# Kernel optimization log

Measured on AMD Instinct MI355X. Metric: run time of the kernel, lower is better.

Reference implementation:

```python
import jax, jax.numpy as jnp
import numpy as np

B, NV, NC, K = 2048, 1000, 4260, 3      # formulas, vars, clauses, literals/clause
NODES = 2 * NV + NC + 1                  # per-sample: pos lits | neg lits | clauses | root
N = B * NODES
C = B * NC


def setup_inputs() -> dict:
    key = jax.random.key(0)
    k1, k2 = jax.random.split(key)
    base = jnp.arange(B, dtype=jnp.int32) * NODES
    # positive / negative literal node ids (neg literal i is nv positions after pos literal i)
    pos_idx = (base[:, None] + jnp.arange(NV, dtype=jnp.int32)).ravel()
    neg_idx = pos_idx + NV
    # each clause picks K random literals from its own sample's 2*NV literal nodes
    lits = jax.random.randint(k1, (B, NC, K), 0, 2 * NV, dtype=jnp.int32)
    or_src = (lits + base[:, None, None]).ravel()              # [E] literal node per OR edge
    or_seg = jnp.repeat(jnp.arange(C, dtype=jnp.int32), K)     # [E] clause id per OR edge
    and_seg = jnp.repeat(jnp.arange(B, dtype=jnp.int32), NC)   # [C] root id per clause
    emb = jax.random.uniform(k2, (N,), dtype=jnp.float32)      # soft assignments in [0,1]
    return {"emb": emb, "pos_idx": pos_idx, "neg_idx": neg_idx,
            "or_src": or_src, "or_seg": or_seg, "and_seg": and_seg,
            "n_clauses": C, "n_roots": B, "epoch": 10}


def reference(emb, pos_idx, neg_idx, or_src, or_seg, and_seg, n_clauses, n_roots, epoch):
    t = jnp.asarray(epoch, jnp.float32) ** (-1.2)  # annealing temperature
    # literal transform: temporary[ind==1] = 1 - emb[ind==0]
    lit = emb.at[neg_idx].set(1.0 - emb[pos_idx])
    # --- OR gates: temperature-scaled soft-max over each clause's literals ---
    v = lit[or_src]                                            # [E] gathered literal values
    m = jax.ops.segment_max(v, or_seg, num_segments=n_clauses)
    w = jnp.exp((v - m[or_seg]) / t)                           # stabilized exp weights
    num = jax.ops.segment_sum(v * w, or_seg, num_segments=n_clauses)
    den = jax.ops.segment_sum(w, or_seg, num_segments=n_clauses)
    clause = num / den                                         # [C] soft-OR per clause
    # --- AND gate: temperature-scaled soft-min over each sample's clauses ---
    mn = jax.ops.segment_min(clause, and_seg, num_segments=n_roots)
    w2 = jnp.exp(-(clause - mn[and_seg]) / t)
    num2 = jax.ops.segment_sum(clause * w2, and_seg, num_segments=n_roots)
    den2 = jax.ops.segment_sum(w2, and_seg, num_segments=n_roots)
    return num2 / den2                                         # [B] soft-SAT per sample
```

## Files before the change

kernel.cpp:

```cpp
#include <hip/hip_runtime.h>

#define TPB 256

struct __align__(4) Int3 { int x, y, z; };

__global__ __launch_bounds__(TPB) void soft_sat_kernel(
    const float* __restrict__ emb,
    const int*   __restrict__ or_src,
    const int*   __restrict__ epoch_p,
    float* __restrict__ out,
    int NV, int NC, int NODES)
{
    extern __shared__ float smem[];
    float* lit = smem;
    float* cls = lit + 2 * NV;
    float* red = cls + NC;

    const int b     = blockIdx.x;
    const int tid   = threadIdx.x;
    const int lane  = tid & 63;
    const int wid   = tid >> 6;
    const int baseI = b * NODES;

    const float invt = powf((float)epoch_p[0], 1.2f);

    const float* embb = emb + baseI;
    for (int i = tid; i < NV; i += TPB) {
        float e = embb[i];
        lit[i]      = e;
        lit[i + NV] = 1.0f - e;
    }
    __syncthreads();

    const Int3* __restrict__ osb = (const Int3*)(or_src + (long long)b * NC * 3);
    float lmin = 3.4e38f;
    for (int c = tid; c < NC; c += TPB) {
        Int3 s = osb[c];
        float v0 = lit[s.x - baseI];
        float v1 = lit[s.y - baseI];
        float v2 = lit[s.z - baseI];
        float m  = fmaxf(fmaxf(v0, v1), v2);
        float w0 = __expf((v0 - m) * invt);
        float w1 = __expf((v1 - m) * invt);
        float w2 = __expf((v2 - m) * invt);
        float num = fmaf(v0, w0, fmaf(v1, w1, v2 * w2));
        float den = w0 + w1 + w2;
        float cv  = num / den;
        cls[c] = cv;
        lmin = fminf(lmin, cv);
    }

    for (int off = 32; off; off >>= 1) lmin = fminf(lmin, __shfl_xor(lmin, off));
    if (lane == 0) red[wid] = lmin;
    __syncthreads();
    if (tid == 0) {
        float m = red[0];
        for (int w = 1; w < TPB / 64; ++w) m = fminf(m, red[w]);
        red[0] = m;
    }
    __syncthreads();
    const float mn = red[0];
    __syncthreads();

    float n2 = 0.0f, d2 = 0.0f;
    for (int c = tid; c < NC; c += TPB) {
        float cv = cls[c];
        float w = __expf((mn - cv) * invt);
        n2 = fmaf(cv, w, n2);
        d2 += w;
    }
    for (int off = 32; off; off >>= 1) {
        n2 += __shfl_xor(n2, off);
        d2 += __shfl_xor(d2, off);
    }
    if (lane == 0) { red[wid] = n2; red[8 + wid] = d2; }
    __syncthreads();
    if (tid == 0) {
        float a = 0.0f, d = 0.0f;
        for (int w = 0; w < TPB / 64; ++w) { a += red[w]; d += red[8 + w]; }
        out[b] = a / d;
    }
}

extern "C" void kernel_launch(void* const* d_in, const int* in_sizes, int n_in,
                              void* d_out, int out_size, void* d_ws, size_t ws_size,
                              hipStream_t stream)
{
    const float* emb     = (const float*)d_in[0];
    const int*   or_src  = (const int*)d_in[3];
    const int*   epoch_p = (const int*)d_in[8];
    float*       out     = (float*)d_out;

    const int B     = out_size;
    const int NV    = in_sizes[1] / B;
    const int NODES = in_sizes[0] / B;
    const int C     = in_sizes[5];
    const int NC    = C / B;

    const size_t smem = (size_t)(2 * NV + NC + 16) * sizeof(float);
    soft_sat_kernel<<<B, TPB, smem, stream>>>(emb, or_src, epoch_p, out,
                                              NV, NC, NODES);
}
```

Measured before the change: 257.6 us.

## Fuse clause soft-OR and root soft-min via online rescaled reduction

```diff
diff --git a/kernel.cpp b/kernel.cpp
--- a/kernel.cpp
+++ b/kernel.cpp
@@ -2,9 +2,16 @@
 
 #define TPB 256
 
-struct __align__(4) Int3 { int x, y, z; };
 
-__global__ __launch_bounds__(TPB) void soft_sat_kernel(
+__device__ __forceinline__ float softor3(float a, float b, float c, float invt) {
+    float m  = fmaxf(fmaxf(a, b), c);
+    float wa = __expf((a - m) * invt);
+    float wb = __expf((b - m) * invt);
+    float wc = __expf((c - m) * invt);
+    return fmaf(a, wa, fmaf(b, wb, c * wc)) / (wa + wb + wc);
+}
+
+__global__ __launch_bounds__(TPB, 8) void soft_sat_kernel(
     const float* __restrict__ emb,
     const int*   __restrict__ or_src,
     const int*   __restrict__ epoch_p,
@@ -13,8 +20,7 @@
 {
     extern __shared__ float smem[];
     float* lit = smem;
-    float* cls = lit + 2 * NV;
-    float* red = cls + NC;
+    float* red = smem + 2 * NV;
 
     const int b     = blockIdx.x;
     const int tid   = threadIdx.x;
@@ -32,53 +38,70 @@
     }
     __syncthreads();
 
-    const Int3* __restrict__ osb = (const Int3*)(or_src + (long long)b * NC * 3);
-    float lmin = 3.4e38f;
-    for (int c = tid; c < NC; c += TPB) {
-        Int3 s = osb[c];
-        float v0 = lit[s.x - baseI];
-        float v1 = lit[s.y - baseI];
-        float v2 = lit[s.z - baseI];
-        float m  = fmaxf(fmaxf(v0, v1), v2);
-        float w0 = __expf((v0 - m) * invt);
-        float w1 = __expf((v1 - m) * invt);
-        float w2 = __expf((v2 - m) * invt);
-        float num = fmaf(v0, w0, fmaf(v1, w1, v2 * w2));
-        float den = w0 + w1 + w2;
-        float cv  = num / den;
-        cls[c] = cv;
-        lmin = fminf(lmin, cv);
+    const int* osb = or_src + (long long)b * NC * 3;
+
+    float mn = 3.4e38f, n2 = 0.0f, d2 = 0.0f;
+
+    int c0 = 0;
+    for (; c0 + TPB * 4 <= NC; c0 += TPB * 4) {
+        const int4* p = (const int4*)(osb + (c0 + tid * 4) * 3);
+        int4 A = p[0], Bv = p[1], Cv = p[2];
+
+        float cv0 = softor3(lit[A.x  - baseI], lit[A.y  - baseI], lit[A.z  - baseI], invt);
+        float cv1 = softor3(lit[A.w  - baseI], lit[Bv.x - baseI], lit[Bv.y - baseI], invt);
+        float cv2 = softor3(lit[Bv.z - baseI], lit[Bv.w - baseI], lit[Cv.x - baseI], invt);
+        float cv3 = softor3(lit[Cv.y - baseI], lit[Cv.z - baseI], lit[Cv.w - baseI], invt);
+
+        float cmin = fminf(fminf(cv0, cv1), fminf(cv2, cv3));
+        float m = fminf(mn, cmin);
+        float f = __expf((m - mn) * invt);
+        n2 *= f; d2 *= f; mn = m;
+
+        float w0 = __expf((mn - cv0) * invt);
+        float w1 = __expf((mn - cv1) * invt);
+        float w2 = __expf((mn - cv2) * invt);
+        float w3 = __expf((mn - cv3) * invt);
+        n2 = fmaf(cv0, w0, fmaf(cv1, w1, fmaf(cv2, w2, fmaf(cv3, w3, n2))));
+        d2 += w0 + w1 + w2 + w3;
     }
 
-    for (int off = 32; off; off >>= 1) lmin = fminf(lmin, __shfl_xor(lmin, off));
-    if (lane == 0) red[wid] = lmin;
-    __syncthreads();
-    if (tid == 0) {
-        float m = red[0];
-        for (int w = 1; w < TPB / 64; ++w) m = fminf(m, red[w]);
-        red[0] = m;
-    }
-    __syncthreads();
-    const float mn = red[0];
-    __syncthreads();
-
-    float n2 = 0.0f, d2 = 0.0f;
-    for (int c = tid; c < NC; c += TPB) {
-        float cv = cls[c];
+    for (int c = c0 + tid; c < NC; c += TPB) {
+        const int* q = osb + c * 3;
+        float cv = softor3(lit[q[0] - baseI], lit[q[1] - baseI], lit[q[2] - baseI], invt);
+        float m = fminf(mn, cv);
+        float f = __expf((m - mn) * invt);
+        n2 *= f; d2 *= f; mn = m;
         float w = __expf((mn - cv) * invt);
         n2 = fmaf(cv, w, n2);
         d2 += w;
     }
+
     for (int off = 32; off; off >>= 1) {
-        n2 += __shfl_xor(n2, off);
-        d2 += __shfl_xor(d2, off);
+        float mo = __shfl_xor(mn, off);
+        float no = __shfl_xor(n2, off);
+        float dd = __shfl_xor(d2, off);
+        float m  = fminf(mn, mo);
+        float f1 = __expf((m - mn) * invt);
+        float f2 = __expf((m - mo) * invt);
+        n2 = n2 * f1 + no * f2;
+        d2 = d2 * f1 + dd * f2;
+        mn = m;
     }
-    if (lane == 0) { red[wid] = n2; red[8 + wid] = d2; }
+    if (lane == 0) { red[wid * 3] = mn; red[wid * 3 + 1] = n2; red[wid * 3 + 2] = d2; }
     __syncthreads();
+
     if (tid == 0) {
-        float a = 0.0f, d = 0.0f;
-        for (int w = 0; w < TPB / 64; ++w) { a += red[w]; d += red[8 + w]; }
-        out[b] = a / d;
+        float M = red[0], N2 = red[1], D2 = red[2];
+        for (int w = 1; w < TPB / 64; ++w) {
+            float mo = red[w * 3], no = red[w * 3 + 1], dd = red[w * 3 + 2];
+            float m  = fminf(M, mo);
+            float f1 = __expf((m - M) * invt);
+            float f2 = __expf((m - mo) * invt);
+            N2 = N2 * f1 + no * f2;
+            D2 = D2 * f1 + dd * f2;
+            M = m;
+        }
+        out[b] = N2 / D2;
     }
 }
 
@@ -97,7 +120,7 @@
     const int C     = in_sizes[5];
     const int NC    = C / B;
 
-    const size_t smem = (size_t)(2 * NV + NC + 16) * sizeof(float);
+    const size_t smem = (size_t)(2 * NV + 12) * sizeof(float);
     soft_sat_kernel<<<B, TPB, smem, stream>>>(emb, or_src, epoch_p, out,
                                               NV, NC, NODES);
 }
```

New measurement: 250.2 us. -2.9%, faster.
